# Performance work log

Measured on AMD Instinct MI355X. Metric: run time of the kernel, lower is better.

## Reference

```python
import jax, jax.numpy as jnp
import numpy as np

B, T, D, S, P, R = 8, 512, 256, 64, 1024, 12


def setup_inputs() -> dict:
    key = jax.random.key(0)
    ks = jax.random.split(key, 8)
    encoded = jax.random.normal(ks[0], (B, T, D), dtype=jnp.float32)
    span_starts = jax.random.randint(ks[1], (B, S), 0, 500).astype(jnp.int32)
    span_lens = jax.random.randint(ks[2], (B, S), 0, 12).astype(jnp.int32)  # end = start + len + 1 <= T
    pair_head = jax.random.randint(ks[3], (B, P), 0, S).astype(jnp.int32)
    pair_tail = jax.random.randint(ks[4], (B, P), 0, S).astype(jnp.int32)
    W_linear = (jax.random.normal(ks[5], (2 * D, R), dtype=jnp.float32) / np.sqrt(2 * D)).astype(jnp.float32)
    b_linear = jnp.zeros((R,), dtype=jnp.float32)
    W_bilinear = (jax.random.normal(ks[6], (R, D, D), dtype=jnp.float32) / D).astype(jnp.float32)
    return dict(encoded=encoded, W_linear=W_linear, b_linear=b_linear, W_bilinear=W_bilinear,
                span_starts=span_starts, span_lens=span_lens, pair_head=pair_head, pair_tail=pair_tail)


def reference(encoded, W_linear, b_linear, W_bilinear, span_starts, span_lens, pair_head, pair_tail):
    # --- ragged span max-pooling (self.pool = max over encoded[b, start:end]) ---
    span_ends = span_starts + span_lens + 1  # exclusive end, length >= 1
    pos = jnp.arange(T)  # [T]
    in_span = (pos[None, None, :] >= span_starts[:, :, None]) & (pos[None, None, :] < span_ends[:, :, None])  # [B,S,T]
    neg_inf = jnp.finfo(encoded.dtype).min
    span_pooled = jnp.max(jnp.where(in_span[..., None], encoded[:, None, :, :], neg_inf), axis=2)  # [B,S,D]

    # --- pair feature gather: [span_pooled[head], span_pooled[tail]] ---
    head = jnp.take_along_axis(span_pooled, pair_head[..., None].astype(jnp.int32), axis=1)  # [B,P,D]
    tail = jnp.take_along_axis(span_pooled, pair_tail[..., None].astype(jnp.int32), axis=1)  # [B,P,D]
    pair_rep = jnp.concatenate([head, tail], axis=-1)  # [B,P,2D]

    # --- linear + bilinear classifier, sigmoid scores ---
    scores = pair_rep @ W_linear + b_linear  # [B,P,R]
    scores = scores + jnp.einsum('bpd,rde,bpe->bpr', head, W_bilinear, tail)
    return jax.nn.sigmoid(scores)
```

## Files before the change

### kernel.cpp

```cpp
#include <hip/hip_runtime.h>
#include <math.h>

#define B 8
#define T 512
#define D 256
#define S 64
#define P 1024
#define R 12

typedef __attribute__((ext_vector_type(8)))  short bf16x8;
typedef __attribute__((ext_vector_type(16))) float f32x16;

static __device__ inline short f2bf(float f) {
    union { float f; unsigned u; } v; v.f = f;
    unsigned u = v.u + 0x7fff + ((v.u >> 16) & 1);
    return (short)(u >> 16);
}

__global__ __launch_bounds__(256) void k_span_pool(
    const float* __restrict__ enc, const int* __restrict__ starts,
    const int* __restrict__ lens, const float* __restrict__ Wl,
    float* __restrict__ sp, short* __restrict__ spb, float* __restrict__ lin)
{
    int bs = blockIdx.x;
    int b  = bs >> 6;
    int d  = threadIdx.x;
    int st = starts[bs];
    int ln = lens[bs];

    const float* base = enc + ((size_t)(b * T + st)) * D + d;
    float m = base[0];
    for (int i = 1; i <= ln; ++i) m = fmaxf(m, base[(size_t)i * D]);
    sp [(size_t)bs * D + d] = m;
    spb[(size_t)bs * D + d] = f2bf(m);

    __shared__ float smem[256];
    smem[d] = m;
    __syncthreads();

    int wave = d >> 6, lane = d & 63;
    #pragma unroll
    for (int oo = 0; oo < 6; ++oo) {
        int o = wave * 6 + oo;
        int r = (o < 12) ? o : (o - 12);
        int rowbase = (o < 12) ? 0 : D;
        float p = 0.f;
        #pragma unroll
        for (int k = 0; k < 4; ++k) {
            int dd = lane + 64 * k;
            p = fmaf(smem[dd], Wl[(size_t)(rowbase + dd) * R + r], p);
        }
        #pragma unroll
        for (int off = 32; off > 0; off >>= 1) p += __shfl_down(p, off, 64);
        if (lane == 0) lin[(size_t)bs * 24 + o] = p;
    }
}

__global__ __launch_bounds__(256) void k_wb_transpose(
    const float* __restrict__ Wb, short* __restrict__ Wt)
{
    int dblk = blockIdx.x;
    int r    = blockIdx.y;
    int e    = threadIdx.x;

    const float* src = Wb + ((size_t)r * D + dblk * 8) * D + e;
    short v[8];
    #pragma unroll
    for (int j = 0; j < 8; ++j) v[j] = f2bf(src[(size_t)j * D]);

    short* dst = Wt + ((size_t)r * D + e) * D + dblk * 8;
    *(bf16x8*)dst = *(bf16x8*)v;
}

__global__ __launch_bounds__(256) void k_bilinear_mfma(
    const short* __restrict__ spb, const short* __restrict__ Wt,
    float* __restrict__ U)
{
    int wave = threadIdx.x >> 6;
    int lane = threadIdx.x & 63;
    int m0 = blockIdx.x * 64 + (wave >> 1) * 32;
    int n0 = blockIdx.y * 64 + (wave & 1) * 32;
    int r  = blockIdx.z;

    int half = lane >> 5;
    int mn   = lane & 31;

    const short* ap = spb + (size_t)(m0 + mn) * D + half * 8;
    const short* bp = Wt + ((size_t)r * D + (n0 + mn)) * D + half * 8;

    f32x16 acc = {};
    #pragma unroll
    for (int ks = 0; ks < 16; ++ks) {
        bf16x8 a = *(const bf16x8*)(ap + ks * 16);
        bf16x8 b = *(const bf16x8*)(bp + ks * 16);
        acc = __builtin_amdgcn_mfma_f32_32x32x16_bf16(a, b, acc, 0, 0, 0);
    }

    #pragma unroll
    for (int reg = 0; reg < 16; ++reg) {
        int m = m0 + (reg & 3) + 8 * (reg >> 2) + 4 * half;
        int n = n0 + mn;
        U[((size_t)m * R + r) * D + n] = acc[reg];
    }
}

__global__ __launch_bounds__(256) void k_scores(
    const float* __restrict__ sp, const float* __restrict__ U,
    const float* __restrict__ lin, const int* __restrict__ ph,
    const int* __restrict__ pt, const float* __restrict__ bl,
    float* __restrict__ out)
{
    int pair = blockIdx.x * 4 + (threadIdx.x >> 6);
    int lane = threadIdx.x & 63;
    int b = pair >> 10;
    int p = pair & 1023;

    int h = ph[(size_t)b * P + p];
    int t = pt[(size_t)b * P + p];

    float4 tv = ((const float4*)(sp + ((size_t)(b * S + t)) * D))[lane];
    const float4* Up = (const float4*)(U + ((size_t)(b * S + h)) * R * D);

    float acc[R];
    #pragma unroll
    for (int r = 0; r < R; ++r) {
        float4 u = Up[r * 64 + lane];
        float a = u.x * tv.x;
        a = fmaf(u.y, tv.y, a);
        a = fmaf(u.z, tv.z, a);
        a = fmaf(u.w, tv.w, a);
        acc[r] = a;
    }
    #pragma unroll
    for (int off = 32; off > 0; off >>= 1) {
        #pragma unroll
        for (int r = 0; r < R; ++r) acc[r] += __shfl_down(acc[r], off, 64);
    }

    if (lane == 0) {
        const float* linH = lin + ((size_t)(b * S + h)) * 24;
        const float* linT = lin + ((size_t)(b * S + t)) * 24;
        #pragma unroll
        for (int r = 0; r < R; ++r) {
            float sc = acc[r] + linH[r] + linT[12 + r] + bl[r];
            out[(size_t)(b * P + p) * R + r] = 1.f / (1.f + expf(-sc));
        }
    }
}

extern "C" void kernel_launch(void* const* d_in, const int* in_sizes, int n_in,
                              void* d_out, int out_size, void* d_ws, size_t ws_size,
                              hipStream_t stream) {
    const float* enc    = (const float*)d_in[0];
    const float* Wl     = (const float*)d_in[1];
    const float* bl     = (const float*)d_in[2];
    const float* Wb     = (const float*)d_in[3];
    const int*   starts = (const int*)d_in[4];
    const int*   lens   = (const int*)d_in[5];
    const int*   ph     = (const int*)d_in[6];
    const int*   pt     = (const int*)d_in[7];
    float* out = (float*)d_out;

    float* sp  = (float*)d_ws;
    float* U   = sp + (size_t)B * S * D;
    float* lin = U + (size_t)B * S * R * D;
    short* spb = (short*)(lin + (size_t)B * S * 24);
    short* Wt  = spb + (size_t)B * S * D;

    k_span_pool    <<<B * S,              256, 0, stream>>>(enc, starts, lens, Wl, sp, spb, lin);
    k_wb_transpose <<<dim3(32, R),        256, 0, stream>>>(Wb, Wt);
    k_bilinear_mfma<<<dim3(8, 4, R),      256, 0, stream>>>(spb, Wt, U);
    k_scores       <<<B * P / 4,          256, 0, stream>>>(sp, U, lin, ph, pt, bl, out);
}
```

Baseline: 101.0 us.

## Merge prep kernels, store bilinear intermediate in bf16, unroll pooling, vectorize output

```diff
diff --git a/kernel.cpp b/kernel.cpp
--- a/kernel.cpp
+++ b/kernel.cpp
@@ -16,65 +16,74 @@
     unsigned u = v.u + 0x7fff + ((v.u >> 16) & 1);
     return (short)(u >> 16);
 }
+static __device__ inline float bf2f(unsigned short h) {
+    union { unsigned u; float f; } v; v.u = ((unsigned)h) << 16;
+    return v.f;
+}
 
-__global__ __launch_bounds__(256) void k_span_pool(
+__global__ __launch_bounds__(256) void k_prep(
     const float* __restrict__ enc, const int* __restrict__ starts,
     const int* __restrict__ lens, const float* __restrict__ Wl,
-    float* __restrict__ sp, short* __restrict__ spb, float* __restrict__ lin)
+    const float* __restrict__ Wb,
+    float* __restrict__ sp, short* __restrict__ spb, float* __restrict__ lin,
+    short* __restrict__ Wt)
 {
-    int bs = blockIdx.x;
-    int b  = bs >> 6;
-    int d  = threadIdx.x;
-    int st = starts[bs];
-    int ln = lens[bs];
+    if (blockIdx.x < B * S) {
+        int bs = blockIdx.x;
+        int b  = bs >> 6;
+        int d  = threadIdx.x;
+        int st = starts[bs];
+        int ln = lens[bs];
 
-    const float* base = enc + ((size_t)(b * T + st)) * D + d;
-    float m = base[0];
-    for (int i = 1; i <= ln; ++i) m = fmaxf(m, base[(size_t)i * D]);
-    sp [(size_t)bs * D + d] = m;
-    spb[(size_t)bs * D + d] = f2bf(m);
+        const float* base = enc + ((size_t)(b * T + st)) * D + d;
+        float m = base[0];
+        #pragma unroll
+        for (int i = 1; i < 12; ++i) {
+            int idx = (i <= ln) ? i : ln;
+            m = fmaxf(m, base[(size_t)idx * D]);
+        }
+        sp [(size_t)bs * D + d] = m;
+        spb[(size_t)bs * D + d] = f2bf(m);
 
-    __shared__ float smem[256];
-    smem[d] = m;
-    __syncthreads();
+        __shared__ float smem[256];
+        smem[d] = m;
+        __syncthreads();
 
-    int wave = d >> 6, lane = d & 63;
-    #pragma unroll
-    for (int oo = 0; oo < 6; ++oo) {
-        int o = wave * 6 + oo;
-        int r = (o < 12) ? o : (o - 12);
-        int rowbase = (o < 12) ? 0 : D;
-        float p = 0.f;
+        int wave = d >> 6, lane = d & 63;
         #pragma unroll
-        for (int k = 0; k < 4; ++k) {
-            int dd = lane + 64 * k;
-            p = fmaf(smem[dd], Wl[(size_t)(rowbase + dd) * R + r], p);
+        for (int oo = 0; oo < 6; ++oo) {
+            int o = wave * 6 + oo;
+            int r = (o < 12) ? o : (o - 12);
+            int rowbase = (o < 12) ? 0 : D;
+            float p = 0.f;
+            #pragma unroll
+            for (int k = 0; k < 4; ++k) {
+                int dd = lane + 64 * k;
+                p = fmaf(smem[dd], Wl[(size_t)(rowbase + dd) * R + r], p);
+            }
+            #pragma unroll
+            for (int off = 32; off > 0; off >>= 1) p += __shfl_down(p, off, 64);
+            if (lane == 0) lin[(size_t)bs * 24 + o] = p;
         }
+    } else {
+        int bid  = blockIdx.x - B * S;
+        int dblk = bid & 31;
+        int r    = bid >> 5;
+        int e    = threadIdx.x;
+
+        const float* src = Wb + ((size_t)r * D + dblk * 8) * D + e;
+        short v[8];
         #pragma unroll
-        for (int off = 32; off > 0; off >>= 1) p += __shfl_down(p, off, 64);
-        if (lane == 0) lin[(size_t)bs * 24 + o] = p;
+        for (int j = 0; j < 8; ++j) v[j] = f2bf(src[(size_t)j * D]);
+
+        short* dst = Wt + ((size_t)r * D + e) * D + dblk * 8;
+        *(bf16x8*)dst = *(bf16x8*)v;
     }
-}
-
-__global__ __launch_bounds__(256) void k_wb_transpose(
-    const float* __restrict__ Wb, short* __restrict__ Wt)
-{
-    int dblk = blockIdx.x;
-    int r    = blockIdx.y;
-    int e    = threadIdx.x;
-
-    const float* src = Wb + ((size_t)r * D + dblk * 8) * D + e;
-    short v[8];
-    #pragma unroll
-    for (int j = 0; j < 8; ++j) v[j] = f2bf(src[(size_t)j * D]);
-
-    short* dst = Wt + ((size_t)r * D + e) * D + dblk * 8;
-    *(bf16x8*)dst = *(bf16x8*)v;
 }
 
 __global__ __launch_bounds__(256) void k_bilinear_mfma(
     const short* __restrict__ spb, const short* __restrict__ Wt,
-    float* __restrict__ U)
+    short* __restrict__ U)
 {
     int wave = threadIdx.x >> 6;
     int lane = threadIdx.x & 63;
@@ -100,12 +109,12 @@
     for (int reg = 0; reg < 16; ++reg) {
         int m = m0 + (reg & 3) + 8 * (reg >> 2) + 4 * half;
         int n = n0 + mn;
-        U[((size_t)m * R + r) * D + n] = acc[reg];
+        U[((size_t)m * R + r) * D + n] = f2bf(acc[reg]);
     }
 }
 
 __global__ __launch_bounds__(256) void k_scores(
-    const float* __restrict__ sp, const float* __restrict__ U,
+    const float* __restrict__ sp, const short* __restrict__ U,
     const float* __restrict__ lin, const int* __restrict__ ph,
     const int* __restrict__ pt, const float* __restrict__ bl,
     float* __restrict__ out)
@@ -119,16 +128,16 @@
     int t = pt[(size_t)b * P + p];
 
     float4 tv = ((const float4*)(sp + ((size_t)(b * S + t)) * D))[lane];
-    const float4* Up = (const float4*)(U + ((size_t)(b * S + h)) * R * D);
+    const ushort4* Up = (const ushort4*)(U + ((size_t)(b * S + h)) * R * D);
 
     float acc[R];
     #pragma unroll
     for (int r = 0; r < R; ++r) {
-        float4 u = Up[r * 64 + lane];
-        float a = u.x * tv.x;
-        a = fmaf(u.y, tv.y, a);
-        a = fmaf(u.z, tv.z, a);
-        a = fmaf(u.w, tv.w, a);
+        ushort4 u = Up[r * 64 + lane];
+        float a = bf2f(u.x) * tv.x;
+        a = fmaf(bf2f(u.y), tv.y, a);
+        a = fmaf(bf2f(u.z), tv.z, a);
+        a = fmaf(bf2f(u.w), tv.w, a);
         acc[r] = a;
     }
     #pragma unroll
@@ -140,11 +149,16 @@
     if (lane == 0) {
         const float* linH = lin + ((size_t)(b * S + h)) * 24;
         const float* linT = lin + ((size_t)(b * S + t)) * 24;
+        float s[R];
         #pragma unroll
         for (int r = 0; r < R; ++r) {
             float sc = acc[r] + linH[r] + linT[12 + r] + bl[r];
-            out[(size_t)(b * P + p) * R + r] = 1.f / (1.f + expf(-sc));
+            s[r] = 1.f / (1.f + expf(-sc));
         }
+        float4* op = (float4*)(out + (size_t)(b * P + p) * R);
+        op[0] = make_float4(s[0], s[1], s[2],  s[3]);
+        op[1] = make_float4(s[4], s[5], s[6],  s[7]);
+        op[2] = make_float4(s[8], s[9], s[10], s[11]);
     }
 }
 
@@ -162,13 +176,12 @@
     float* out = (float*)d_out;
 
     float* sp  = (float*)d_ws;
-    float* U   = sp + (size_t)B * S * D;
-    float* lin = U + (size_t)B * S * R * D;
+    float* lin = sp + (size_t)B * S * D;
     short* spb = (short*)(lin + (size_t)B * S * 24);
-    short* Wt  = spb + (size_t)B * S * D;
+    short* U   = spb + (size_t)B * S * D;
+    short* Wt  = U + (size_t)B * S * R * D;
 
-    k_span_pool    <<<B * S,              256, 0, stream>>>(enc, starts, lens, Wl, sp, spb, lin);
-    k_wb_transpose <<<dim3(32, R),        256, 0, stream>>>(Wb, Wt);
-    k_bilinear_mfma<<<dim3(8, 4, R),      256, 0, stream>>>(spb, Wt, U);
-    k_scores       <<<B * P / 4,          256, 0, stream>>>(sp, U, lin, ph, pt, bl, out);
+    k_prep         <<<B * S + 32 * R, 256, 0, stream>>>(enc, starts, lens, Wl, Wb, sp, spb, lin, Wt);
+    k_bilinear_mfma<<<dim3(8, 4, R),  256, 0, stream>>>(spb, Wt, U);
+    k_scores       <<<B * P / 4,      256, 0, stream>>>(sp, U, lin, ph, pt, bl, out);
 }
```

After: 97.03 us. 4.0% less time.
